# Kernel optimization log

Hardware: AMD Instinct MI355X
Metric: run time of the kernel (lower is better)

Reference implementation:

```python
import jax, jax.numpy as jnp
import numpy as np
import math

B, H, W, CV = 8, 128, 128, 256
T, CT = 77, 512
HEADS, HEAD_DIM = 8, 32
TOP_M = 5
LN_EPS = 1e-5
NORM_EPS = 1e-6
CLAMP = 2.0


def _ln(x, w, b):
    mu = jnp.mean(x, axis=-1, keepdims=True)
    var = jnp.mean(jnp.square(x - mu), axis=-1, keepdims=True)
    return (x - mu) * jax.lax.rsqrt(var + LN_EPS) * w + b


def _l2norm(x):
    n = jnp.sqrt(jnp.sum(jnp.square(x), axis=-1, keepdims=True))
    return x / jnp.maximum(n, NORM_EPS)


def setup_inputs() -> dict:
    key = jax.random.key(0)
    ks = jax.random.split(key, 12)
    s = 0.02
    return {
        "visual_features": jax.random.normal(ks[0], (B, H, W, CV), jnp.float32),
        "text_features": jax.random.normal(ks[1], (B, T, CT), jnp.float32),
        "norm1_w": jnp.ones((CV,), jnp.float32),
        "norm1_b": jnp.zeros((CV,), jnp.float32),
        "q_w": s * jax.random.normal(ks[2], (CV, CV), jnp.float32),
        "q_b": jnp.zeros((CV,), jnp.float32),
        "k_w": s * jax.random.normal(ks[3], (CT, CV), jnp.float32),
        "k_b": jnp.zeros((CV,), jnp.float32),
        "v_w": s * jax.random.normal(ks[4], (CT, CV), jnp.float32),
        "v_b": jnp.zeros((CV,), jnp.float32),
        "out_w": s * jax.random.normal(ks[5], (CV, CV), jnp.float32),
        "out_b": jnp.zeros((CV,), jnp.float32),
        "gate_w": s * jax.random.normal(ks[6], (CV, 1), jnp.float32),
        "gate_b": jnp.zeros((1,), jnp.float32),
        "logit_scale": jnp.asarray(math.log(1.0 / 0.07), jnp.float32),
        "alpha": jnp.asarray(0.1, jnp.float32),
        "norm2_w": jnp.ones((CV,), jnp.float32),
        "norm2_b": jnp.zeros((CV,), jnp.float32),
        "ffn1_w": s * jax.random.normal(ks[7], (CV, 4 * CV), jnp.float32),
        "ffn1_b": jnp.zeros((4 * CV,), jnp.float32),
        "ffn2_w": s * jax.random.normal(ks[8], (4 * CV, CV), jnp.float32),
        "ffn2_b": jnp.zeros((CV,), jnp.float32),
    }


def reference(visual_features, text_features, norm1_w, norm1_b, q_w, q_b, k_w, k_b,
              v_w, v_b, out_w, out_b, gate_w, gate_b, logit_scale, alpha,
              norm2_w, norm2_b, ffn1_w, ffn1_b, ffn2_w, ffn2_b):
    b, h, w, cv = visual_features.shape
    n = h * w
    # Pre-LN then flatten spatial dims: (B, N, Cv)
    x = _ln(visual_features, norm1_w, norm1_b).reshape(b, n, cv)
    q_full = x @ q_w + q_b                      # (B, N, Cv)
    k_full = text_features @ k_w + k_b          # (B, T, Cv)
    v_full = text_features @ v_w + v_b          # (B, T, Cv)
    # padding mask: all-zero text tokens
    pad = jnp.sum(jnp.abs(text_features), axis=-1) <= 1e-6  # (B, T)
    # cosine-normalize over FULL Cv dim, then split heads
    q = _l2norm(q_full).reshape(b, n, HEADS, HEAD_DIM)
    k = _l2norm(k_full).reshape(b, -1, HEADS, HEAD_DIM)
    v = v_full.reshape(b, -1, HEADS, HEAD_DIM)
    scale = jnp.exp(jnp.clip(logit_scale, -CLAMP, CLAMP)) / jnp.sqrt(jnp.float32(HEAD_DIM))
    sim = jnp.einsum('bnhd,bthd->bnht', q, k) * scale  # (B, N, Hh, T)
    sim = jnp.where(pad[:, None, None, :], -jnp.inf, sim)
    # top-k pruning over text tokens (threshold at k-th value; ties measure-zero)
    topv = jax.lax.top_k(sim, TOP_M)[0]
    sim = jnp.where(sim >= topv[..., -1:], sim, -jnp.inf)
    attn = jax.nn.softmax(sim, axis=-1)
    aligned = jnp.einsum('bnht,bthd->bnhd', attn, v).reshape(b, n, cv)
    aligned = aligned @ out_w + out_b
    gate = jax.nn.sigmoid(x @ gate_w + gate_b)  # (B, N, 1)
    y = x + alpha * gate * aligned
    y = _ln(y, norm2_w, norm2_b)
    ffn = jax.nn.gelu(y @ ffn1_w + ffn1_b, approximate=False) @ ffn2_w + ffn2_b
    y = y + ffn
    return y.reshape(b, h, w, cv)
```

## Files before the change

kernel.cpp:

```cpp
#include <hip/hip_runtime.h>
#include <hip/hip_bf16.h>

typedef _Float16 h16;
typedef __attribute__((ext_vector_type(8))) _Float16 halfx8;
typedef __attribute__((ext_vector_type(4))) _Float16 halfx4;
typedef __attribute__((ext_vector_type(4))) float f32x4;

__device__ __forceinline__ void gload_lds16(const void* g, void* l) {
  __builtin_amdgcn_global_load_lds((const __attribute__((address_space(1))) unsigned int*)g,
                                   (__attribute__((address_space(3))) unsigned int*)l, 16, 0, 0);
}
__device__ __forceinline__ unsigned umax_(unsigned a, unsigned b) { return a > b ? a : b; }
__device__ __forceinline__ unsigned umin_(unsigned a, unsigned b) { return a < b ? a : b; }

__device__ __forceinline__ float fast_gelu(float v) {
  float x2 = v * v;
  float w_ = v * fmaf(x2, 0.0713548163f, 1.5957691216f);
  float e = __expf(w_);
  float r = 1.f / (1.f + e);
  return v * e * r;
}

__global__ __launch_bounds__(256) void conv_all_kernel(
    const float* __restrict__ qw, const float* __restrict__ ow,
    const float* __restrict__ f1w, const float* __restrict__ f2w,
    h16* __restrict__ qwT, h16* __restrict__ owT,
    h16* __restrict__ f1T, h16* __restrict__ f2T)
{
  int bid = blockIdx.x, tid = threadIdx.x;
  const float* in; h16* out; int logN, K, base;
  if (bid < 256)       { in = qw;  out = qwT; logN = 8;  K = 256;  base = 0; }
  else if (bid < 512)  { in = ow;  out = owT; logN = 8;  K = 256;  base = 256; }
  else if (bid < 1536) { in = f1w; out = f1T; logN = 10; K = 256;  base = 512; }
  else                 { in = f2w; out = f2T; logN = 8;  K = 1024; base = 1536; }
  int idx = (bid - base) * 256 + tid;
  int k = idx >> logN, n = idx & ((1 << logN) - 1);
  out[(size_t)n * K + k] = (h16)in[idx];
}

__global__ __launch_bounds__(256) void text_kv_kernel(const float* __restrict__ tf,
    const float* __restrict__ kw, const float* __restrict__ kb,
    const float* __restrict__ vw, const float* __restrict__ vb,
    const float* __restrict__ lsp,
    h16* __restrict__ ko, h16* __restrict__ vo, float* __restrict__ padf)
{
  __shared__ h16 st[4 * 512];
  __shared__ float kro[4 * 256];
  __shared__ float ssc[4];
  int bx = blockIdx.x, b = bx / 20, tg = bx % 20, t0 = tg * 4;
  int tid = threadIdx.x, lane = tid & 63, wid = tid >> 6;
  for (int i = tid; i < 4 * 512; i += 256) {
    int tl = i >> 9, j = i & 511, t = t0 + tl;
    float v = (t < 77) ? tf[((size_t)b * 77 + t) * 512 + j] : 0.f;
    st[i] = (h16)v;
  }
  __syncthreads();
  {
    int t = t0 + wid;
    float a = 0.f;
    #pragma unroll
    for (int j = 0; j < 8; j++) a += fabsf((float)st[wid * 512 + lane + j * 64]);
    #pragma unroll
    for (int o = 32; o; o >>= 1) a += __shfl_xor(a, o);
    if (lane == 0) padf[b * 80 + t] = (a <= 1e-6f) ? -1e30f : 0.f;
  }
  int c = tid;
  float kacc[4], vacc[4];
  #pragma unroll
  for (int tl = 0; tl < 4; tl++) { kacc[tl] = kb[c]; vacc[tl] = vb[c]; }
  for (int j = 0; j < 512; j++) {
    float wkv = kw[(size_t)j * 256 + c];
    float wvv = vw[(size_t)j * 256 + c];
    #pragma unroll
    for (int tl = 0; tl < 4; tl++) {
      float x = (float)st[tl * 512 + j];
      kacc[tl] += x * wkv; vacc[tl] += x * wvv;
    }
  }
  #pragma unroll
  for (int tl = 0; tl < 4; tl++) kro[tl * 256 + c] = kacc[tl] * kacc[tl];
  __syncthreads();
  {
    float s2 = kro[wid * 256 + lane] + kro[wid * 256 + lane + 64]
             + kro[wid * 256 + lane + 128] + kro[wid * 256 + lane + 192];
    #pragma unroll
    for (int o = 32; o; o >>= 1) s2 += __shfl_xor(s2, o);
    if (lane == 0) {
      float ls = lsp[0];
      float scale = __expf(fminf(fmaxf(ls, -2.f), 2.f)) * rsqrtf(32.f);
      ssc[wid] = scale / fmaxf(sqrtf(s2), 1e-6f);
    }
  }
  __syncthreads();
  int h = c >> 5, d = c & 31, g = d >> 3, e = d & 7;
  #pragma unroll
  for (int tl = 0; tl < 4; tl++) {
    int t = t0 + tl;
    int kt = t >> 4, l15 = t & 15, ln = g * 16 + l15;
    size_t koff = ((((size_t)(b * 8 + h) * 5 + kt) * 64) + ln) * 8 + e;
    size_t voff = (((size_t)(b * 8 + h) * 80) + t) * 32 + d;
    ko[koff] = (t < 77) ? (h16)(kacc[tl] * ssc[tl]) : (h16)0.f;
    vo[voff] = (t < 77) ? (h16)vacc[tl] : (h16)0.f;
  }
}

__global__ __launch_bounds__(256) void ln1_kernel(const float* __restrict__ vis,
    const float* __restrict__ w, const float* __restrict__ bia,
    const float* __restrict__ gw, const float* __restrict__ gb,
    h16* __restrict__ x, float* __restrict__ gate)
{
  int lane = threadIdx.x & 63;
  size_t row = (size_t)blockIdx.x * 4 + (threadIdx.x >> 6);
  const float4 v = ((const float4*)(vis + row * 256))[lane];
  float s = v.x + v.y + v.z + v.w;
  float q = v.x * v.x + v.y * v.y + v.z * v.z + v.w * v.w;
  #pragma unroll
  for (int o = 32; o; o >>= 1) { s += __shfl_xor(s, o); q += __shfl_xor(q, o); }
  float mean = s * (1.f / 256.f);
  float rstd = rsqrtf(q * (1.f / 256.f) - mean * mean + 1e-5f);
  float4 wv = ((const float4*)w)[lane], bv = ((const float4*)bia)[lane];
  float x0 = (v.x - mean) * rstd * wv.x + bv.x;
  float x1 = (v.y - mean) * rstd * wv.y + bv.y;
  float x2 = (v.z - mean) * rstd * wv.z + bv.z;
  float x3 = (v.w - mean) * rstd * wv.w + bv.w;
  float4 gv = ((const float4*)gw)[lane];
  float g = x0 * gv.x + x1 * gv.y + x2 * gv.z + x3 * gv.w;
  #pragma unroll
  for (int o = 32; o; o >>= 1) g += __shfl_xor(g, o);
  if (lane == 0) gate[row] = 1.f / (1.f + __expf(-(g + gb[0])));
  halfx4 o4; o4[0] = (h16)x0; o4[1] = (h16)x1; o4[2] = (h16)x2; o4[3] = (h16)x3;
  ((halfx4*)(x + row * 256))[lane] = o4;
}

__global__ __launch_bounds__(256) void gemmQ_kernel(const h16* __restrict__ A,
    const h16* __restrict__ Wt, const float* __restrict__ bias, h16* __restrict__ outp)
{
  __shared__ char sA[8192];
  __shared__ char sB[32768];
  int m0 = blockIdx.x * 64;
  int tid = threadIdx.x, lane = tid & 63, wid = tid >> 6;
  int wn = wid;
  int l15 = lane & 15, l4 = lane >> 4, xk = l15 & 7;
  f32x4 acc[4][4];
  #pragma unroll
  for (int a = 0; a < 4; a++)
    #pragma unroll
    for (int b2 = 0; b2 < 4; b2++) acc[a][b2] = (f32x4){0.f, 0.f, 0.f, 0.f};
  const size_t sa = 512;
  int srow = lane >> 3;
  int scol = ((lane & 7) ^ srow) * 16;
  const char* Ab = (const char*)A + (size_t)m0 * sa + scol;
  const char* Bb = (const char*)Wt + scol;
  for (int k0 = 0; k0 < 256; k0 += 64) {
    #pragma unroll
    for (int cc = 0; cc < 2; cc++) {
      int ch = wid * 2 + cc;
      gload_lds16(Ab + (size_t)(ch * 8 + srow) * sa + k0 * 2, sA + ch * 1024);
    }
    #pragma unroll
    for (int cc = 0; cc < 8; cc++) {
      int ch = wid * 8 + cc;
      gload_lds16(Bb + (size_t)(ch * 8 + srow) * sa + k0 * 2, sB + ch * 1024);
    }
    asm volatile("s_waitcnt vmcnt(0)" ::: "memory");
    __syncthreads();
    #pragma unroll
    for (int ks = 0; ks < 2; ks++) {
      halfx8 af[4], bf[4];
      #pragma unroll
      for (int f = 0; f < 4; f++) {
        af[f] = *(const halfx8*)(sA + (f * 16 + l15) * 128 + (((ks * 4 + l4) ^ xk) * 16));
        bf[f] = *(const halfx8*)(sB + (wn * 64 + f * 16 + l15) * 128 + (((ks * 4 + l4) ^ xk) * 16));
      }
      #pragma unroll
      for (int fm = 0; fm < 4; fm++)
        #pragma unroll
        for (int fn = 0; fn < 4; fn++)
          acc[fm][fn] = __builtin_amdgcn_mfma_f32_16x16x32_f16(af[fm], bf[fn], acc[fm][fn], 0, 0, 0);
    }
    __syncthreads();
  }
  float bv[4];
  #pragma unroll
  for (int fn = 0; fn < 4; fn++) bv[fn] = bias[wn * 64 + fn * 16 + l15];
  float ps[4][4];
  #pragma unroll
  for (int fm = 0; fm < 4; fm++)
    #pragma unroll
    for (int r = 0; r < 4; r++) {
      float s = 0.f;
      #pragma unroll
      for (int fn = 0; fn < 4; fn++) {
        float v = acc[fm][fn][r] + bv[fn];
        acc[fm][fn][r] = v;
        s += v * v;
      }
      ps[fm][r] = s;
    }
  #pragma unroll
  for (int o = 1; o <= 8; o <<= 1)
    #pragma unroll
    for (int fm = 0; fm < 4; fm++)
      #pragma unroll
      for (int r = 0; r < 4; r++) ps[fm][r] += __shfl_xor(ps[fm][r], o);
  if (l15 == 0) {
    #pragma unroll
    for (int fm = 0; fm < 4; fm++)
      #pragma unroll
      for (int r = 0; r < 4; r++)
        ((float*)sA)[(fm * 16 + l4 * 4 + r) * 4 + wn] = ps[fm][r];
  }
  __syncthreads();
  #pragma unroll
  for (int fm = 0; fm < 4; fm++)
    #pragma unroll
    for (int r = 0; r < 4; r++) {
      const float* p = (const float*)sA + (fm * 16 + l4 * 4 + r) * 4;
      float S = p[0] + p[1] + p[2] + p[3];
      float sc = 1.f / fmaxf(sqrtf(S), 1e-6f);
      size_t row = (size_t)(m0 + fm * 16 + l4 * 4 + r);
      #pragma unroll
      for (int fn = 0; fn < 4; fn++)
        outp[row * 256 + wn * 64 + fn * 16 + l15] = (h16)(acc[fm][fn][r] * sc);
    }
}

__global__ __launch_bounds__(256) void gemmO_kernel(const h16* __restrict__ A,
    const h16* __restrict__ Wt, const float* __restrict__ ob,
    const h16* __restrict__ x, const float* __restrict__ gate,
    const float* __restrict__ alphap, const float* __restrict__ w2,
    const float* __restrict__ b2, h16* __restrict__ outp)
{
  __shared__ char sA[8192];
  __shared__ char sB[32768];
  int m0 = blockIdx.x * 64;
  int tid = threadIdx.x, lane = tid & 63, wid = tid >> 6;
  int wn = wid;
  int l15 = lane & 15, l4 = lane >> 4, xk = l15 & 7;
  f32x4 acc[4][4];
  #pragma unroll
  for (int a = 0; a < 4; a++)
    #pragma unroll
    for (int b2_ = 0; b2_ < 4; b2_++) acc[a][b2_] = (f32x4){0.f, 0.f, 0.f, 0.f};
  const size_t sa = 512;
  int srow = lane >> 3;
  int scol = ((lane & 7) ^ srow) * 16;
  const char* Ab = (const char*)A + (size_t)m0 * sa + scol;
  const char* Bb = (const char*)Wt + scol;
  for (int k0 = 0; k0 < 256; k0 += 64) {
    #pragma unroll
    for (int cc = 0; cc < 2; cc++) {
      int ch = wid * 2 + cc;
      gload_lds16(Ab + (size_t)(ch * 8 + srow) * sa + k0 * 2, sA + ch * 1024);
    }
    #pragma unroll
    for (int cc = 0; cc < 8; cc++) {
      int ch = wid * 8 + cc;
      gload_lds16(Bb + (size_t)(ch * 8 + srow) * sa + k0 * 2, sB + ch * 1024);
    }
    asm volatile("s_waitcnt vmcnt(0)" ::: "memory");
    __syncthreads();
    #pragma unroll
    for (int ks = 0; ks < 2; ks++) {
      halfx8 af[4], bf[4];
      #pragma unroll
      for (int f = 0; f < 4; f++) {
        af[f] = *(const halfx8*)(sA + (f * 16 + l15) * 128 + (((ks * 4 + l4) ^ xk) * 16));
        bf[f] = *(const halfx8*)(sB + (wn * 64 + f * 16 + l15) * 128 + (((ks * 4 + l4) ^ xk) * 16));
      }
      #pragma unroll
      for (int fm = 0; fm < 4; fm++)
        #pragma unroll
        for (int fn = 0; fn < 4; fn++)
          acc[fm][fn] = __builtin_amdgcn_mfma_f32_16x16x32_f16(af[fm], bf[fn], acc[fm][fn], 0, 0, 0);
    }
    __syncthreads();
  }
  float bv[4], w2v[4], b2v[4];
  #pragma unroll
  for (int fn = 0; fn < 4; fn++) {
    int col = wn * 64 + fn * 16 + l15;
    bv[fn] = ob[col]; w2v[fn] = w2[col]; b2v[fn] = b2[col];
  }
  float al = alphap[0];
  float s1[4][4], s2[4][4];
  #pragma unroll
  for (int fm = 0; fm < 4; fm++)
    #pragma unroll
    for (int r = 0; r < 4; r++) {
      size_t row = (size_t)(m0 + fm * 16 + l4 * 4 + r);
      float ga = al * gate[row];
      float a1 = 0.f, a2 = 0.f;
      #pragma unroll
      for (int fn = 0; fn < 4; fn++) {
        float v = acc[fm][fn][r] + bv[fn];
        float xv = (float)x[row * 256 + wn * 64 + fn * 16 + l15];
        float y = xv + ga * v;
        acc[fm][fn][r] = y;
        a1 += y; a2 += y * y;
      }
      s1[fm][r] = a1; s2[fm][r] = a2;
    }
  #pragma unroll
  for (int o = 1; o <= 8; o <<= 1)
    #pragma unroll
    for (int fm = 0; fm < 4; fm++)
      #pragma unroll
      for (int r = 0; r < 4; r++) {
        s1[fm][r] += __shfl_xor(s1[fm][r], o);
        s2[fm][r] += __shfl_xor(s2[fm][r], o);
      }
  if (l15 == 0) {
    #pragma unroll
    for (int fm = 0; fm < 4; fm++)
      #pragma unroll
      for (int r = 0; r < 4; r++) {
        int rr = fm * 16 + l4 * 4 + r;
        ((float*)sA)[rr * 8 + wn * 2 + 0] = s1[fm][r];
        ((float*)sA)[rr * 8 + wn * 2 + 1] = s2[fm][r];
      }
  }
  __syncthreads();
  #pragma unroll
  for (int fm = 0; fm < 4; fm++)
    #pragma unroll
    for (int r = 0; r < 4; r++) {
      int rr = fm * 16 + l4 * 4 + r;
      const float* p = (const float*)sA + rr * 8;
      float S1 = p[0] + p[2] + p[4] + p[6];
      float S2 = p[1] + p[3] + p[5] + p[7];
      float mean = S1 * (1.f / 256.f);
      float var = S2 * (1.f / 256.f) - mean * mean;
      float rstd = rsqrtf(var + 1e-5f);
      size_t row = (size_t)(m0 + rr);
      #pragma unroll
      for (int fn = 0; fn < 4; fn++) {
        float y = acc[fm][fn][r];
        outp[row * 256 + wn * 64 + fn * 16 + l15] =
            (h16)((y - mean) * rstd * w2v[fn] + b2v[fn]);
      }
    }
}

__global__ __launch_bounds__(512, 2) void ffn_fused_kernel(
    const h16* __restrict__ y2g, const h16* __restrict__ w1t, const float* __restrict__ b1,
    const h16* __restrict__ w2t, const float* __restrict__ b2, float* __restrict__ outp)
{
  __shared__ char smem[81920];
  char* sW1 = smem;
  char* sW2 = smem + 32768;
  char* sH  = smem + 65536;
  float* sE = (float*)smem;

  int m0 = blockIdx.x * 128;
  int tid = threadIdx.x, lane = tid & 63, wid = tid >> 6;
  int l15 = lane & 15, l4 = lane >> 4;
  int wm1 = wid >> 1, wn1 = wid & 1;
  int wm2 = wid >> 2, wn2 = wid & 3;

  halfx8 afy[2][8];
  #pragma unroll
  for (int fm = 0; fm < 2; fm++) {
    size_t row = (size_t)(m0 + wm1 * 32 + fm * 16 + l15);
    #pragma unroll
    for (int ks = 0; ks < 8; ks++)
      afy[fm][ks] = *(const halfx8*)&y2g[row * 256 + ks * 32 + l4 * 8];
  }

  f32x4 acc2[4][4];
  #pragma unroll
  for (int a = 0; a < 4; a++)
    #pragma unroll
    for (int b_ = 0; b_ < 4; b_++) acc2[a][b_] = (f32x4){0.f, 0.f, 0.f, 0.f};

  for (int c = 0; c < 16; c++) {
    float b1v0 = b1[c * 64 + wn1 * 32 + l15];
    float b1v1 = b1[c * 64 + wn1 * 32 + 16 + l15];
    #pragma unroll
    for (int j = 0; j < 4; j++) {
      int i = j * 512 + tid;
      int r = i >> 5, g = i & 31;
      gload_lds16(w1t + (size_t)(c * 64 + r) * 256 + ((g ^ (r & 7)) * 8),
                  sW1 + (j * 512 + wid * 64) * 16);
    }
    #pragma unroll
    for (int j = 0; j < 4; j++) {
      int i = j * 512 + tid;
      int r = i >> 3, g = i & 7;
      gload_lds16(w2t + (size_t)r * 1024 + c * 64 + ((g ^ (r & 7)) * 8),
                  sW2 + (j * 512 + wid * 64) * 16);
    }
    asm volatile("s_waitcnt vmcnt(0)" ::: "memory");
    __syncthreads();
    f32x4 a1[2][2];
    #pragma unroll
    for (int a = 0; a < 2; a++)
      #pragma unroll
      for (int b_ = 0; b_ < 2; b_++) a1[a][b_] = (f32x4){0.f, 0.f, 0.f, 0.f};
    #pragma unroll
    for (int ks = 0; ks < 8; ks++) {
      #pragma unroll
      for (int fc = 0; fc < 2; fc++) {
        int nrow = wn1 * 32 + fc * 16 + l15;
        halfx8 bf = *(const halfx8*)(sW1 + (size_t)nrow * 512 + (((ks * 4 + l4) ^ (nrow & 7)) * 16));
        #pragma unroll
        for (int fm = 0; fm < 2; fm++)
          a1[fm][fc] = __builtin_amdgcn_mfma_f32_16x16x32_f16(afy[fm][ks], bf, a1[fm][fc], 0, 0, 0);
      }
    }
    #pragma unroll
    for (int fm = 0; fm < 2; fm++)
      #pragma unroll
      for (int fc = 0; fc < 2; fc++)
        #pragma unroll
        for (int r = 0; r < 4; r++) {
          int row = wm1 * 32 + fm * 16 + l4 * 4 + r;
          int col = wn1 * 32 + fc * 16 + l15;
          float v = fast_gelu(a1[fm][fc][r] + (fc ? b1v1 : b1v0));
          ((h16*)(sH + row * 128 + (((col >> 3) ^ (row & 7)) * 16)))[col & 7] = (h16)v;
        }
    __syncthreads();
    #pragma unroll
    for (int ks = 0; ks < 2; ks++) {
      halfx8 ah[4], bw[4];
      #pragma unroll
      for (int f = 0; f < 4; f++) {
        int hrow = wm2 * 64 + f * 16 + l15;
        ah[f] = *(const halfx8*)(sH + hrow * 128 + (((ks * 4 + l4) ^ (hrow & 7)) * 16));
        int wrow = wn2 * 64 + f * 16 + l15;
        bw[f] = *(const halfx8*)(sW2 + (size_t)wrow * 128 + (((ks * 4 + l4) ^ (wrow & 7)) * 16));
      }
      #pragma unroll
      for (int fm = 0; fm < 4; fm++)
        #pragma unroll
        for (int fn = 0; fn < 4; fn++)
          acc2[fm][fn] = __builtin_amdgcn_mfma_f32_16x16x32_f16(ah[fm], bw[fn], acc2[fm][fn], 0, 0, 0);
    }
    __syncthreads();
  }

  int rowl = tid >> 3, cg = tid & 7;
  #pragma unroll
  for (int half = 0; half < 2; half++) {
    if (wm2 == half) {
      #pragma unroll
      for (int fm = 0; fm < 4; fm++)
        #pragma unroll
        for (int fn = 0; fn < 4; fn++)
          #pragma unroll
          for (int r = 0; r < 4; r++)
            sE[(fm * 16 + l4 * 4 + r) * 264 + wn2 * 64 + fn * 16 + l15] = acc2[fm][fn][r];
    }
    __syncthreads();
    size_t grow = (size_t)(m0 + half * 64 + rowl);
    #pragma unroll
    for (int k = 0; k < 8; k++) {
      int c0 = cg * 4 + k * 32;
      float4 v = *(float4*)&sE[rowl * 264 + c0];
      halfx4 rv = *(const halfx4*)&y2g[grow * 256 + c0];
      float4 bb = *(const float4*)&b2[c0];
      float4 o;
      o.x = v.x + (float)rv[0] + bb.x;
      o.y = v.y + (float)rv[1] + bb.y;
      o.z = v.z + (float)rv[2] + bb.z;
      o.w = v.w + (float)rv[3] + bb.w;
      *(float4*)&outp[grow * 256 + c0] = o;
    }
    __syncthreads();
  }
}

__global__ __launch_bounds__(256) void attn_kernel(const h16* __restrict__ q,
    const h16* __restrict__ kk,
    const h16* __restrict__ vv,
    const float* __restrict__ padf,
    h16* __restrict__ outp)
{
  int bx = blockIdx.x;
  int wid = threadIdx.x >> 6, lane = threadIdx.x & 63;
  int l15 = lane & 15, g = lane >> 4;
  int b = bx >> 8;
  size_t qrow = (size_t)bx * 64 + wid * 16 + l15;
  int base4 = g * 4;
  float pad4[5][4];
  #pragma unroll
  for (int kt = 0; kt < 5; kt++) {
    float4 p4 = *(const float4*)&padf[b * 80 + kt * 16 + base4];
    pad4[kt][0] = p4.x; pad4[kt][1] = p4.y; pad4[kt][2] = p4.z; pad4[kt][3] = p4.w;
  }
  const h16* qp = &q[qrow * 256 + g * 8];
  h16* op = &outp[qrow * 256 + g * 8];
  #pragma unroll 2
  for (int h = 0; h < 8; h++) {
    int ho = h * 32;
    halfx8 qf = *(const halfx8*)(qp + ho);
    const h16* kph = kk + (((size_t)(b * 8 + h) * 5) * 64 + lane) * 8;
    const h16* vph = vv + ((size_t)(b * 8 + h) * 80) * 32 + g * 8;
    f32x4 acc[5];
    #pragma unroll
    for (int kt = 0; kt < 5; kt++) {
      halfx8 kf = *(const halfx8*)(kph + kt * 512);
      acc[kt] = __builtin_amdgcn_mfma_f32_16x16x32_f16(kf, qf, (f32x4){0.f, 0.f, 0.f, 0.f}, 0, 0, 0);
    }
    unsigned pv0 = 0u, pv1 = 0u, pv2 = 0u, pv3 = 0u, pv4 = 0u;
    #pragma unroll
    for (int kt = 0; kt < 5; kt++) {
      #pragma unroll
      for (int r = 0; r < 4; r++) {
        float s = acc[kt][r] + pad4[kt][r];
        int bi = __float_as_int(s);
        unsigned u = ((unsigned)(bi ^ ((bi >> 31) | (int)0x80000000)) & 0xFFFFFF80u)
                   | (unsigned)(base4 + kt * 16 + r);
        unsigned a;
        a = umax_(pv0, u); u = umin_(pv0, u); pv0 = a;
        a = umax_(pv1, u); u = umin_(pv1, u); pv1 = a;
        a = umax_(pv2, u); u = umin_(pv2, u); pv2 = a;
        a = umax_(pv3, u); u = umin_(pv3, u); pv3 = a;
        pv4 = umax_(pv4, u);
      }
    }
    #pragma unroll
    for (int mrd = 0; mrd < 2; mrd++) {
      int msk = mrd ? 32 : 16;
      unsigned b0 = (unsigned)__shfl_xor((int)pv0, msk);
      unsigned b1 = (unsigned)__shfl_xor((int)pv1, msk);
      unsigned b2 = (unsigned)__shfl_xor((int)pv2, msk);
      unsigned b3 = (unsigned)__shfl_xor((int)pv3, msk);
      unsigned b4 = (unsigned)__shfl_xor((int)pv4, msk);
      unsigned c0 = umax_(pv0, b0);
      unsigned c1 = umax_(umax_(umin_(pv0, b0), pv1), b1);
      unsigned c2 = umax_(umax_(umin_(pv0, b1), umin_(pv1, b0)), umax_(pv2, b2));
      unsigned c3 = umax_(umax_(umax_(umin_(pv0, b2), umin_(pv1, b1)), umin_(pv2, b0)), umax_(pv3, b3));
      unsigned c4 = umax_(umax_(umax_(umin_(pv0, b3), umin_(pv1, b2)),
                                umax_(umin_(pv2, b1), umin_(pv3, b0))), umax_(pv4, b4));
      pv0 = c0; pv1 = c1; pv2 = c2; pv3 = c3; pv4 = c4;
    }
    unsigned pvs[5] = {pv0, pv1, pv2, pv3, pv4};
    float pw[5]; int ti[5]; float den = 0.f;
    #pragma unroll
    for (int k = 0; k < 5; k++) {
      unsigned u = pvs[k];
      int sg = ((int)u) >> 31;
      float tv = __int_as_float(u ^ (0x80000000u | (unsigned)~sg));
      ti[k] = (int)(u & 0x7Fu);
      pw[k] = __expf(tv);
      den += pw[k];
    }
    float inv = 1.f / den;
    halfx8 o8 = {};
    #pragma unroll
    for (int k = 0; k < 5; k++) {
      h16 ph = (h16)(pw[k] * inv);
      halfx8 v = *(const halfx8*)(vph + ti[k] * 32);
      halfx8 p8 = {ph, ph, ph, ph, ph, ph, ph, ph};
      o8 = o8 + p8 * v;
    }
    *(halfx8*)(op + ho) = o8;
  }
}

extern "C" void kernel_launch(void* const* d_in, const int* in_sizes, int n_in,
                              void* d_out, int out_size, void* d_ws, size_t ws_size,
                              hipStream_t stream)
{
  const float* vis = (const float*)d_in[0];
  const float* tf  = (const float*)d_in[1];
  const float* n1w = (const float*)d_in[2];
  const float* n1b = (const float*)d_in[3];
  const float* qw  = (const float*)d_in[4];
  const float* qb  = (const float*)d_in[5];
  const float* kw  = (const float*)d_in[6];
  const float* kb  = (const float*)d_in[7];
  const float* vw  = (const float*)d_in[8];
  const float* vb  = (const float*)d_in[9];
  const float* ow  = (const float*)d_in[10];
  const float* ob  = (const float*)d_in[11];
  const float* gw  = (const float*)d_in[12];
  const float* gb  = (const float*)d_in[13];
  const float* ls  = (const float*)d_in[14];
  const float* al  = (const float*)d_in[15];
  const float* n2w = (const float*)d_in[16];
  const float* n2b = (const float*)d_in[17];
  const float* f1w = (const float*)d_in[18];
  const float* f1b = (const float*)d_in[19];
  const float* f2w = (const float*)d_in[20];
  const float* f2b = (const float*)d_in[21];

  char* ws = (char*)d_ws;
  const size_t MB_ = 1024ull * 1024ull;
  h16*  kS   = (h16*)(ws + 0 * MB_);
  h16*  vS   = (h16*)(ws + 1 * MB_);
  float* padf = (float*)(ws + 2 * MB_);
  float* gate = (float*)(ws + 3 * MB_);
  h16*  qwT  = (h16*)(ws + 4 * MB_);
  h16*  owT  = (h16*)(ws + 5 * MB_);
  h16*  f1T  = (h16*)(ws + 6 * MB_);
  h16*  f2T  = (h16*)(ws + 7 * MB_);
  h16*  xh   = (h16*)(ws + 16 * MB_);
  h16*  qh   = (h16*)(ws + 80 * MB_);
  h16*  alg  = (h16*)(ws + 144 * MB_);

  conv_all_kernel<<<2560, 256, 0, stream>>>(qw, ow, f1w, f2w, qwT, owT, f1T, f2T);

  text_kv_kernel<<<160, 256, 0, stream>>>(tf, kw, kb, vw, vb, ls, kS, vS, padf);
  ln1_kernel<<<32768, 256, 0, stream>>>(vis, n1w, n1b, gw, gb, xh, gate);

  gemmQ_kernel<<<2048, 256, 0, stream>>>(xh, qwT, qb, qh);

  attn_kernel<<<2048, 256, 0, stream>>>(qh, kS, vS, padf, qh);

  gemmO_kernel<<<2048, 256, 0, stream>>>(qh, owT, ob, xh, gate, al, n2w, n2b, alg);

  ffn_fused_kernel<<<1024, 512, 0, stream>>>(alg, f1T, f1b, f2T, f2b, (float*)d_out);
}
```

Before: 560.1 us.

## Double-buffer FFN weight tiles in LDS and prefetch next chunk

```diff
diff --git a/kernel.cpp b/kernel.cpp
--- a/kernel.cpp
+++ b/kernel.cpp
@@ -342,14 +342,33 @@
     }
 }
 
+__device__ __forceinline__ void ffn_stage(const h16* __restrict__ w1t,
+                                          const h16* __restrict__ w2t,
+                                          int c, char* dW1, char* dW2, int tid, int wid)
+{
+  #pragma unroll
+  for (int j = 0; j < 4; j++) {
+    int i = j * 512 + tid;
+    int r = i >> 5, g = i & 31;
+    gload_lds16(w1t + (size_t)(c * 64 + r) * 256 + ((g ^ (r & 7)) * 8),
+                dW1 + (j * 512 + wid * 64) * 16);
+  }
+  #pragma unroll
+  for (int j = 0; j < 4; j++) {
+    int i = j * 512 + tid;
+    int r = i >> 3, g = i & 7;
+    gload_lds16(w2t + (size_t)r * 1024 + c * 64 + ((g ^ (r & 7)) * 8),
+                dW2 + (j * 512 + wid * 64) * 16);
+  }
+}
+
 __global__ __launch_bounds__(512, 2) void ffn_fused_kernel(
     const h16* __restrict__ y2g, const h16* __restrict__ w1t, const float* __restrict__ b1,
     const h16* __restrict__ w2t, const float* __restrict__ b2, float* __restrict__ outp)
 {
-  __shared__ char smem[81920];
-  char* sW1 = smem;
-  char* sW2 = smem + 32768;
-  char* sH  = smem + 65536;
+  __shared__ char smem[151552];
+  char* sH = smem + 131072;
+  float* sB1 = (float*)(smem + 147456);
   float* sE = (float*)smem;
 
   int m0 = blockIdx.x * 128;
@@ -358,6 +377,8 @@
   int wm1 = wid >> 1, wn1 = wid & 1;
   int wm2 = wid >> 2, wn2 = wid & 3;
 
+  ((float2*)sB1)[tid] = ((const float2*)b1)[tid];
+
   halfx8 afy[2][8];
   #pragma unroll
   for (int fm = 0; fm < 2; fm++) {
@@ -373,30 +394,32 @@
     #pragma unroll
     for (int b_ = 0; b_ < 4; b_++) acc2[a][b_] = (f32x4){0.f, 0.f, 0.f, 0.f};
 
+  ffn_stage(w1t, w2t, 0, smem, smem + 65536, tid, wid);
+  asm volatile("s_waitcnt lgkmcnt(0)" ::: "memory");
+
   for (int c = 0; c < 16; c++) {
-    float b1v0 = b1[c * 64 + wn1 * 32 + l15];
-    float b1v1 = b1[c * 64 + wn1 * 32 + 16 + l15];
-    #pragma unroll
-    for (int j = 0; j < 4; j++) {
-      int i = j * 512 + tid;
-      int r = i >> 5, g = i & 31;
-      gload_lds16(w1t + (size_t)(c * 64 + r) * 256 + ((g ^ (r & 7)) * 8),
-                  sW1 + (j * 512 + wid * 64) * 16);
-    }
-    #pragma unroll
-    for (int j = 0; j < 4; j++) {
-      int i = j * 512 + tid;
-      int r = i >> 3, g = i & 7;
-      gload_lds16(w2t + (size_t)r * 1024 + c * 64 + ((g ^ (r & 7)) * 8),
-                  sW2 + (j * 512 + wid * 64) * 16);
-    }
-    asm volatile("s_waitcnt vmcnt(0)" ::: "memory");
-    __syncthreads();
+    int buf = c & 1;
+    char* sW1 = smem + buf * 32768;
+    char* sW2 = smem + 65536 + buf * 32768;
+    if (c < 15) {
+      ffn_stage(w1t, w2t, c + 1, smem + (buf ^ 1) * 32768,
+                smem + 65536 + (buf ^ 1) * 32768, tid, wid);
+      asm volatile("s_waitcnt vmcnt(8)" ::: "memory");
+    } else {
+      asm volatile("s_waitcnt vmcnt(0)" ::: "memory");
+    }
+    __builtin_amdgcn_s_barrier();
+    asm volatile("" ::: "memory");
+
+    float b1v0 = sB1[c * 64 + wn1 * 32 + l15];
+    float b1v1 = sB1[c * 64 + wn1 * 32 + 16 + l15];
+
     f32x4 a1[2][2];
     #pragma unroll
     for (int a = 0; a < 2; a++)
       #pragma unroll
       for (int b_ = 0; b_ < 2; b_++) a1[a][b_] = (f32x4){0.f, 0.f, 0.f, 0.f};
+    __builtin_amdgcn_s_setprio(1);
     #pragma unroll
     for (int ks = 0; ks < 8; ks++) {
       #pragma unroll
@@ -408,6 +431,7 @@
           a1[fm][fc] = __builtin_amdgcn_mfma_f32_16x16x32_f16(afy[fm][ks], bf, a1[fm][fc], 0, 0, 0);
       }
     }
+    __builtin_amdgcn_s_setprio(0);
     #pragma unroll
     for (int fm = 0; fm < 2; fm++)
       #pragma unroll
@@ -419,7 +443,10 @@
           float v = fast_gelu(a1[fm][fc][r] + (fc ? b1v1 : b1v0));
           ((h16*)(sH + row * 128 + (((col >> 3) ^ (row & 7)) * 16)))[col & 7] = (h16)v;
         }
-    __syncthreads();
+    asm volatile("s_waitcnt lgkmcnt(0)" ::: "memory");
+    __builtin_amdgcn_s_barrier();
+    asm volatile("" ::: "memory");
+    __builtin_amdgcn_s_setprio(1);
     #pragma unroll
     for (int ks = 0; ks < 2; ks++) {
       halfx8 ah[4], bw[4];
@@ -436,7 +463,10 @@
         for (int fn = 0; fn < 4; fn++)
           acc2[fm][fn] = __builtin_amdgcn_mfma_f32_16x16x32_f16(ah[fm], bw[fn], acc2[fm][fn], 0, 0, 0);
     }
-    __syncthreads();
+    __builtin_amdgcn_s_setprio(0);
+    asm volatile("" ::: "memory");
+    __builtin_amdgcn_s_barrier();
+    asm volatile("" ::: "memory");
   }
 
   int rowl = tid >> 3, cg = tid & 7;
```

New measurement: 550.9 us. About the same (-1.6%).

## Load FFN weights directly from global memory and halve block tile to 64 rows

Applied to the files above, without the earlier changes.

```diff
diff --git a/kernel.cpp b/kernel.cpp
--- a/kernel.cpp
+++ b/kernel.cpp
@@ -342,21 +342,19 @@
     }
 }
 
-__global__ __launch_bounds__(512, 2) void ffn_fused_kernel(
+__global__ __launch_bounds__(256, 2) void ffn_fused_kernel(
     const h16* __restrict__ y2g, const h16* __restrict__ w1t, const float* __restrict__ b1,
     const h16* __restrict__ w2t, const float* __restrict__ b2, float* __restrict__ outp)
 {
-  __shared__ char smem[81920];
-  char* sW1 = smem;
-  char* sW2 = smem + 32768;
-  char* sH  = smem + 65536;
+  __shared__ char smem[67584];
+  char* sH = smem;
   float* sE = (float*)smem;
 
-  int m0 = blockIdx.x * 128;
+  int m0 = blockIdx.x * 64;
   int tid = threadIdx.x, lane = tid & 63, wid = tid >> 6;
   int l15 = lane & 15, l4 = lane >> 4;
   int wm1 = wid >> 1, wn1 = wid & 1;
-  int wm2 = wid >> 2, wn2 = wid & 3;
+  int wn2 = wid;
 
   halfx8 afy[2][8];
   #pragma unroll
@@ -372,26 +370,15 @@
   for (int a = 0; a < 4; a++)
     #pragma unroll
     for (int b_ = 0; b_ < 4; b_++) acc2[a][b_] = (f32x4){0.f, 0.f, 0.f, 0.f};
+
+  const h16* w1base = w1t + (size_t)(wn1 * 32 + l15) * 256 + l4 * 8;
+  const h16* w2base = w2t + (size_t)(wn2 * 64 + l15) * 1024 + l4 * 8;
 
   for (int c = 0; c < 16; c++) {
     float b1v0 = b1[c * 64 + wn1 * 32 + l15];
     float b1v1 = b1[c * 64 + wn1 * 32 + 16 + l15];
-    #pragma unroll
-    for (int j = 0; j < 4; j++) {
-      int i = j * 512 + tid;
-      int r = i >> 5, g = i & 31;
-      gload_lds16(w1t + (size_t)(c * 64 + r) * 256 + ((g ^ (r & 7)) * 8),
-                  sW1 + (j * 512 + wid * 64) * 16);
-    }
-    #pragma unroll
-    for (int j = 0; j < 4; j++) {
-      int i = j * 512 + tid;
-      int r = i >> 3, g = i & 7;
-      gload_lds16(w2t + (size_t)r * 1024 + c * 64 + ((g ^ (r & 7)) * 8),
-                  sW2 + (j * 512 + wid * 64) * 16);
-    }
-    asm volatile("s_waitcnt vmcnt(0)" ::: "memory");
-    __syncthreads();
+    const h16* w1p = w1base + (size_t)(c * 64) * 256;
+
     f32x4 a1[2][2];
     #pragma unroll
     for (int a = 0; a < 2; a++)
@@ -401,13 +388,13 @@
     for (int ks = 0; ks < 8; ks++) {
       #pragma unroll
       for (int fc = 0; fc < 2; fc++) {
-        int nrow = wn1 * 32 + fc * 16 + l15;
-        halfx8 bf = *(const halfx8*)(sW1 + (size_t)nrow * 512 + (((ks * 4 + l4) ^ (nrow & 7)) * 16));
+        halfx8 bf = *(const halfx8*)(w1p + (size_t)(fc * 16) * 256 + ks * 32);
         #pragma unroll
         for (int fm = 0; fm < 2; fm++)
           a1[fm][fc] = __builtin_amdgcn_mfma_f32_16x16x32_f16(afy[fm][ks], bf, a1[fm][fc], 0, 0, 0);
       }
     }
+
     #pragma unroll
     for (int fm = 0; fm < 2; fm++)
       #pragma unroll
@@ -419,16 +406,19 @@
           float v = fast_gelu(a1[fm][fc][r] + (fc ? b1v1 : b1v0));
           ((h16*)(sH + row * 128 + (((col >> 3) ^ (row & 7)) * 16)))[col & 7] = (h16)v;
         }
-    __syncthreads();
+    asm volatile("s_waitcnt lgkmcnt(0)" ::: "memory");
+    __builtin_amdgcn_s_barrier();
+    asm volatile("" ::: "memory");
+
+    const h16* w2p = w2base + c * 64;
     #pragma unroll
     for (int ks = 0; ks < 2; ks++) {
       halfx8 ah[4], bw[4];
       #pragma unroll
       for (int f = 0; f < 4; f++) {
-        int hrow = wm2 * 64 + f * 16 + l15;
+        int hrow = f * 16 + l15;
         ah[f] = *(const halfx8*)(sH + hrow * 128 + (((ks * 4 + l4) ^ (hrow & 7)) * 16));
-        int wrow = wn2 * 64 + f * 16 + l15;
-        bw[f] = *(const halfx8*)(sW2 + (size_t)wrow * 128 + (((ks * 4 + l4) ^ (wrow & 7)) * 16));
+        bw[f] = *(const halfx8*)(w2p + (size_t)(f * 16) * 1024 + ks * 32);
       }
       #pragma unroll
       for (int fm = 0; fm < 4; fm++)
@@ -436,26 +426,25 @@
         for (int fn = 0; fn < 4; fn++)
           acc2[fm][fn] = __builtin_amdgcn_mfma_f32_16x16x32_f16(ah[fm], bw[fn], acc2[fm][fn], 0, 0, 0);
     }
-    __syncthreads();
-  }
-
-  int rowl = tid >> 3, cg = tid & 7;
-  #pragma unroll
-  for (int half = 0; half < 2; half++) {
-    if (wm2 == half) {
-      #pragma unroll
-      for (int fm = 0; fm < 4; fm++)
-        #pragma unroll
-        for (int fn = 0; fn < 4; fn++)
-          #pragma unroll
-          for (int r = 0; r < 4; r++)
-            sE[(fm * 16 + l4 * 4 + r) * 264 + wn2 * 64 + fn * 16 + l15] = acc2[fm][fn][r];
-    }
-    __syncthreads();
-    size_t grow = (size_t)(m0 + half * 64 + rowl);
-    #pragma unroll
-    for (int k = 0; k < 8; k++) {
-      int c0 = cg * 4 + k * 32;
+    asm volatile("s_waitcnt lgkmcnt(0)" ::: "memory");
+    __builtin_amdgcn_s_barrier();
+    asm volatile("" ::: "memory");
+  }
+
+  #pragma unroll
+  for (int fm = 0; fm < 4; fm++)
+    #pragma unroll
+    for (int fn = 0; fn < 4; fn++)
+      #pragma unroll
+      for (int r = 0; r < 4; r++)
+        sE[(fm * 16 + l4 * 4 + r) * 264 + wn2 * 64 + fn * 16 + l15] = acc2[fm][fn][r];
+  __syncthreads();
+  {
+    int rowl = tid >> 2, cg = tid & 3;
+    size_t grow = (size_t)(m0 + rowl);
+    #pragma unroll
+    for (int k = 0; k < 16; k++) {
+      int c0 = cg * 4 + k * 16;
       float4 v = *(float4*)&sE[rowl * 264 + c0];
       halfx4 rv = *(const halfx4*)&y2g[grow * 256 + c0];
       float4 bb = *(const float4*)&b2[c0];
@@ -466,7 +455,6 @@
       o.w = v.w + (float)rv[3] + bb.w;
       *(float4*)&outp[grow * 256 + c0] = o;
     }
-    __syncthreads();
   }
 }
 
@@ -611,5 +599,5 @@
 
   gemmO_kernel<<<2048, 256, 0, stream>>>(qh, owT, ob, xh, gate, al, n2w, n2b, alg);
 
-  ffn_fused_kernel<<<1024, 512, 0, stream>>>(alg, f1T, f1b, f2T, f2b, (float*)d_out);
-}
+  ffn_fused_kernel<<<2048, 256, 0, stream>>>(alg, f1T, f1b, f2T, f2b, (float*)d_out);
+}
```

Result: slower. 764.0 us (+36.4%).
